# Optimization experiments

Hardware: AMD Instinct MI355X
Metric: run time of the kernel (lower is better)

The kernel has to match this reference:

```python
import jax, jax.numpy as jnp
import numpy as np

HID = 100  # LSTM hidden size (fixed in module)


def _lstm_final(x, Wih, Whh, bih, bhh, reverse):
    # x: [N, T, Hin]; returns final hidden state [N, HID] (PyTorch gate order i,f,g,o)
    xs = jnp.flip(x, axis=1) if reverse else x
    pre = jnp.einsum('nth,gh->ntg', xs, Wih) + bih + bhh  # [N, T, 4*HID]
    N = x.shape[0]
    h0 = jnp.zeros((N, HID), x.dtype)
    c0 = jnp.zeros((N, HID), x.dtype)

    def step(carry, pt):
        h, c = carry
        g = pt + h @ Whh.T
        i, f, gg, o = jnp.split(g, 4, axis=-1)
        c = jax.nn.sigmoid(f) * c + jax.nn.sigmoid(i) * jnp.tanh(gg)
        h = jax.nn.sigmoid(o) * jnp.tanh(c)
        return (h, c), None

    (h, c), _ = jax.lax.scan(step, (h0, c0), jnp.swapaxes(pre, 0, 1))
    return h


def setup_inputs():
    key = jax.random.key(0)
    ks = jax.random.split(key, 16)
    H, B, S, NP, PL = 768, 40, 128, 100, 20
    w = lambda k, shape: jax.random.normal(k, shape, jnp.float32) * 0.02
    return {
        'bert_output': jax.random.normal(ks[0], (B, S, H), jnp.float32),
        'commonsense': jax.random.normal(ks[1], (B * NP, PL, H), jnp.float32),
        'attention_mask': jnp.ones((B, S), jnp.int32),
        'commonsense_mask': jnp.ones((B, NP), jnp.int32),
        'b_size': 8, 'num_cand': 5, 'num_path': NP, 'path_len': PL,
        'lstm_Wih_f': w(ks[2], (4 * HID, H)), 'lstm_Whh_f': w(ks[3], (4 * HID, HID)),
        'lstm_bih_f': jnp.zeros((4 * HID,), jnp.float32), 'lstm_bhh_f': jnp.zeros((4 * HID,), jnp.float32),
        'lstm_Wih_b': w(ks[4], (4 * HID, H)), 'lstm_Whh_b': w(ks[5], (4 * HID, HID)),
        'lstm_bih_b': jnp.zeros((4 * HID,), jnp.float32), 'lstm_bhh_b': jnp.zeros((4 * HID,), jnp.float32),
        'proj_W': w(ks[6], (H, 2 * HID)), 'proj_b': jnp.zeros((H,), jnp.float32),
        'W1_w': w(ks[7], (1, H)), 'W1_b': jnp.zeros((1,), jnp.float32),
        'W2_w': w(ks[8], (1, H)), 'W2_b': jnp.zeros((1,), jnp.float32),
        'W3': w(ks[9], (1, 1, H)),
        'attp_W': w(ks[10], (H, 4 * H)), 'attp_b': jnp.zeros((H,), jnp.float32),
        'ln_w': jnp.ones((H,), jnp.float32), 'ln_b': jnp.zeros((H,), jnp.float32),
    }


def reference(bert_output, commonsense, attention_mask, commonsense_mask,
              b_size, num_cand, num_path, path_len,
              lstm_Wih_f, lstm_Whh_f, lstm_bih_f, lstm_bhh_f,
              lstm_Wih_b, lstm_Whh_b, lstm_bih_b, lstm_bhh_b,
              proj_W, proj_b, W1_w, W1_b, W2_w, W2_b, W3,
              attp_W, attp_b, ln_w, ln_b):
    Bc = b_size * num_cand
    # bidirectional LSTM over commonsense paths; only final hidden states are used
    h_f = _lstm_final(commonsense, lstm_Wih_f, lstm_Whh_f, lstm_bih_f, lstm_bhh_f, False)
    h_b = _lstm_final(commonsense, lstm_Wih_b, lstm_Whh_b, lstm_bih_b, lstm_bhh_b, True)
    enc = jnp.concatenate([h_f, h_b], axis=-1)               # [Bc*NP, 200]
    cs = jax.nn.relu(enc @ proj_W.T + proj_b).reshape(Bc, num_path, -1)  # [B, P, H]
    # trilinear BiDAF-style scores
    part1 = bert_output @ W1_w.T + W1_b                      # [B, S, 1]
    part2 = (cs @ W2_w.T + W2_b).transpose(0, 2, 1)          # [B, 1, P]
    part3 = jnp.einsum('bsh,bph->bsp', W3 * bert_output, cs)  # [B, S, P]
    mask_cs = (1.0 - commonsense_mask.astype(jnp.float32)) * -10000.0
    mask_dqa = (1.0 - attention_mask.astype(jnp.float32)) * -10000.0
    total = part1 + part2 + part3 + mask_cs[:, None, :] + mask_dqa[:, :, None]
    cs_att = jax.nn.softmax(total, axis=-1)                  # over paths
    weight_cs = jnp.einsum('bsp,bph->bsh', cs_att, cs)
    ctx_att = jax.nn.softmax(total, axis=1)                  # over context tokens
    probs = jnp.einsum('bsp,btp->bst', cs_att, ctx_att)      # [B, S, S]
    weighted_context = jnp.einsum('bst,bth->bsh', probs, bert_output)
    cat = jnp.concatenate([bert_output, weight_cs, bert_output * weight_cs,
                           bert_output * weighted_context], axis=-1)
    x = jax.nn.relu(cat @ attp_W.T + attp_b) + bert_output
    u = x.mean(-1, keepdims=True)
    s = ((x - u) ** 2).mean(-1, keepdims=True)
    return ln_w * ((x - u) / jnp.sqrt(s + 1e-12)) + ln_b
```

## Files before the change

### kernel.cpp

```cpp
#include <hip/hip_runtime.h>


typedef unsigned short ushort_t;
typedef unsigned int u32;
typedef __attribute__((ext_vector_type(8))) short short8;
typedef __attribute__((ext_vector_type(4))) float f32x4;
typedef __attribute__((address_space(1))) const u32 gu32;
typedef __attribute__((address_space(3))) u32 lu32;

__device__ __forceinline__ ushort_t f2bf(float f) {
  u32 x = __builtin_bit_cast(u32, f);
  u32 r = (x + 0x7fffu + ((x >> 16) & 1u)) >> 16;
  return (ushort_t)r;
}
__device__ __forceinline__ float bflo(u32 u) { return __builtin_bit_cast(float, u << 16); }
__device__ __forceinline__ float bfhi(u32 u) { return __builtin_bit_cast(float, u & 0xffff0000u); }
__device__ __forceinline__ u32 cvtpk(float lo, float hi) {
  u32 r;
  asm("v_cvt_pk_bf16_f32 %0, %1, %2" : "=v"(r) : "v"(lo), "v"(hi));
  return r;
}

__device__ __forceinline__ float sigm(float x) { return 1.f / (1.f + __expf(-x)); }
__device__ __forceinline__ float tanh_f(float x) { return 1.f - 2.f / (__expf(2.f * x) + 1.f); }


__global__ void prep_weights(const float* __restrict__ Wih_f, const float* __restrict__ Wih_b,
                             const float* __restrict__ Whh_f, const float* __restrict__ Whh_b,
                             const float* __restrict__ bih_f, const float* __restrict__ bhh_f,
                             const float* __restrict__ bih_b, const float* __restrict__ bhh_b,
                             const float* __restrict__ projW, const float* __restrict__ attpW,
                             ushort_t* __restrict__ wihcat, ushort_t* __restrict__ whhcat,
                             float* __restrict__ biascat, ushort_t* __restrict__ projw_bf,
                             ushort_t* __restrict__ attpw_bf) {
  const int TOT = 614400 + 102400 + 800 + 196608 + 2359296;
  for (int idx = blockIdx.x * 256 + threadIdx.x; idx < TOT; idx += gridDim.x * 256) {
    if (idx < 614400) {
      int g = idx / 768, k = idx % 768;
      float v = g < 400 ? Wih_f[g * 768 + k] : Wih_b[(g - 400) * 768 + k];
      wihcat[idx] = f2bf(v);
    } else if (idx < 716800) {
      int e = idx - 614400; int g = e / 128, j = e % 128;
      float v = 0.f;
      if (j < 100) v = g < 400 ? Whh_f[g * 100 + j] : Whh_b[(g - 400) * 100 + j];
      whhcat[e] = f2bf(v);
    } else if (idx < 717600) {
      int g = idx - 716800;
      biascat[g] = g < 400 ? bih_f[g] + bhh_f[g] : bih_b[g - 400] + bhh_b[g - 400];
    } else if (idx < 914208) {
      int e = idx - 717600; int o = e / 256, j = e % 256;
      float v = 0.f;
      if (j < 100) v = projW[o * 200 + j];
      else if (j >= 128 && j < 228) v = projW[o * 200 + 100 + (j - 128)];
      projw_bf[e] = f2bf(v);
    } else {
      int e = idx - 914208;
      attpw_bf[e] = f2bf(attpW[e]);
    }
  }
}

__global__ void convert_x_t(const float4* __restrict__ x4, ushort_t* __restrict__ xb) {
  for (int i = blockIdx.x * 256 + threadIdx.x; i < 15360000; i += gridDim.x * 256) {
    int seq = i / 3840;
    int rem = i - seq * 3840;
    int t = rem / 192;
    int k4 = rem - t * 192;
    float4 v = x4[i];
    ushort4 o;
    o.x = f2bf(v.x); o.y = f2bf(v.y); o.z = f2bf(v.z); o.w = f2bf(v.w);
    *reinterpret_cast<ushort4*>(&xb[((size_t)t * 4000 + seq) * 768 + k4 * 4]) = o;
  }
}

__global__ __launch_bounds__(256) void prep_bert(const float* __restrict__ bert,
                                                 const float* __restrict__ W3,
                                                 ushort_t* __restrict__ bw3,
                                                 ushort_t* __restrict__ bT,
                                                 ushort_t* __restrict__ cat) {
  __shared__ ushort_t tl[64 * 130];
  int ht = blockIdx.x, b = blockIdx.y;
  int h0 = ht * 64, tid = threadIdx.x;
  for (int e = tid; e < 8192; e += 256) {
    int t = e >> 6, hh = e & 63;
    float v = bert[((size_t)b * 128 + t) * 768 + h0 + hh];
    ushort_t vb = f2bf(v);
    bw3[((size_t)b * 128 + t) * 768 + h0 + hh] = f2bf(v * W3[h0 + hh]);
    cat[((size_t)b * 128 + t) * 3072 + h0 + hh] = vb;
    tl[hh * 130 + t] = vb;
  }
  __syncthreads();
  for (int e = tid; e < 8192; e += 256) {
    int hh = e >> 7, t = e & 127;
    bT[((size_t)b * 768 + h0 + hh) * 128 + t] = tl[hh * 130 + t];
  }
}

__global__ __launch_bounds__(256) void csT_k(const ushort_t* __restrict__ csb,
                                             ushort_t* __restrict__ csTcat) {
  __shared__ ushort_t tl[64 * 130];
  int ht = blockIdx.x, b = blockIdx.y;
  int h0 = ht * 64, tid = threadIdx.x;
  for (int e = tid; e < 6400; e += 256) {
    int p = e >> 6, hh = e & 63;
    tl[hh * 130 + p] = csb[((size_t)b * 100 + p) * 768 + h0 + hh];
  }
  __syncthreads();
  for (int e = tid; e < 8192; e += 256) {
    int hh = e >> 7, p = e & 127;
    csTcat[((size_t)b * 896 + h0 + hh) * 128 + p] = (p < 100) ? tl[hh * 130 + p] : (ushort_t)0;
  }
}


__global__ __launch_bounds__(256) void gemm_pre160(
    const ushort_t* __restrict__ A,
    const ushort_t* __restrict__ B,
    const float* __restrict__ bias,
    ushort_t* __restrict__ P)
{
  __shared__ __align__(16) ushort_t lsA[128 * 64];
  __shared__ __align__(16) ushort_t lsB[160 * 64];
  int bid = blockIdx.x;
  int xcd = bid & 7, slot = bid >> 3;
  int L = (xcd < 5) ? xcd * 391 + slot : 1955 + (xcd - 5) * 390 + slot;
  int bm = L / 5, bn = L - bm * 5;
  int m0 = bm * 128, n0 = bn * 160;
  int tid = threadIdx.x, lane = tid & 63, w = tid >> 6;
  int wr = w >> 1, wc = w & 1;
  int l15 = lane & 15, lk = lane >> 4;
  f32x4 acc[4][5];
  #pragma unroll
  for (int i = 0; i < 4; ++i)
    #pragma unroll
    for (int j = 0; j < 5; ++j)
      #pragma unroll
      for (int r = 0; r < 4; ++r) acc[i][j][r] = 0.f;

  int r_in = lane >> 3, p = lane & 7;
  for (int kt = 0; kt < 12; ++kt) {
    __syncthreads();
    #pragma unroll
    for (int i = 0; i < 4; ++i) {
      int seg = w * 4 + i;
      int row = seg * 8 + r_in;
      int sl = p ^ (row & 7);
      __builtin_amdgcn_global_load_lds(
          (gu32*)(A + (size_t)(m0 + row) * 768 + kt * 64 + sl * 8),
          (lu32*)(lsA + seg * 512), 16, 0, 0);
    }
    #pragma unroll
    for (int i = 0; i < 5; ++i) {
      int seg = w * 5 + i;
      int row = seg * 8 + r_in;
      int sl = p ^ (row & 7);
      __builtin_amdgcn_global_load_lds(
          (gu32*)(B + (size_t)(n0 + row) * 768 + kt * 64 + sl * 8),
          (lu32*)(lsB + seg * 512), 16, 0, 0);
    }
    __syncthreads();
    #pragma unroll
    for (int ks = 0; ks < 2; ++ks) {
      short8 af[4], bfv[5];
      #pragma unroll
      for (int f = 0; f < 4; ++f) {
        int row = wr * 64 + f * 16 + l15;
        af[f] = *reinterpret_cast<const short8*>(
            &lsA[row * 64 + (((ks * 4 + lk) ^ (row & 7)) << 3)]);
      }
      #pragma unroll
      for (int f = 0; f < 5; ++f) {
        int rowb = wc * 80 + f * 16 + l15;
        bfv[f] = *reinterpret_cast<const short8*>(
            &lsB[rowb * 64 + (((ks * 4 + lk) ^ (rowb & 7)) << 3)]);
      }
      #pragma unroll
      for (int fm = 0; fm < 4; ++fm)
        #pragma unroll
        for (int fn = 0; fn < 5; ++fn)
          acc[fm][fn] = __builtin_amdgcn_mfma_f32_16x16x32_bf16(af[fm], bfv[fn], acc[fm][fn], 0, 0, 0);
    }
  }
  #pragma unroll
  for (int fm = 0; fm < 4; ++fm) {
    int mb = m0 + wr * 64 + fm * 16;
    int t = mb / 4000;
    int sq = mb - t * 4000;
    int cch = sq >> 4;
    #pragma unroll
    for (int fn = 0; fn < 5; ++fn) {
      int nb = n0 + wc * 80 + fn * 16;
      int nl = nb < 400 ? nb : nb - 400;
      int nq = (nb < 400 ? 0 : 25) + (nl >> 4);
      float bsv = bias[nb + l15];
      uint2 pk;
      pk.x = cvtpk(acc[fm][fn][0] + bsv, acc[fm][fn][1] + bsv);
      pk.y = cvtpk(acc[fm][fn][2] + bsv, acc[fm][fn][3] + bsv);
      *reinterpret_cast<uint2*>(
          &P[((((size_t)t * 250 + cch) * 50 + nq) << 8) + l15 * 16 + lk * 4]) = pk;
    }
  }
}


__global__ __launch_bounds__(256) void gemm_proj(
    const ushort_t* __restrict__ A, int lda,
    const ushort_t* __restrict__ B, int ldb,
    int M, int N, int KT,
    const float* __restrict__ bias,
    float* __restrict__ C, int ldc,
    ushort_t* __restrict__ C2)
{
  __shared__ __align__(16) ushort_t lsA[128 * 64];
  __shared__ __align__(16) ushort_t lsB[128 * 64];
  int bm = blockIdx.x, bn = blockIdx.y;
  int m0 = bm * 128, n0 = bn * 128;
  int tid = threadIdx.x, lane = tid & 63, w = tid >> 6;
  int wr = w >> 1, wc = w & 1;
  int l15 = lane & 15, lk = lane >> 4;
  f32x4 acc[4][4];
  #pragma unroll
  for (int i = 0; i < 4; ++i)
    #pragma unroll
    for (int j = 0; j < 4; ++j)
      #pragma unroll
      for (int r = 0; r < 4; ++r) acc[i][j][r] = 0.f;

  int r_in = lane >> 3, p = lane & 7;
  for (int kt = 0; kt < KT; ++kt) {
    __syncthreads();
    #pragma unroll
    for (int i = 0; i < 4; ++i) {
      int seg = w * 4 + i;
      int row = seg * 8 + r_in;
      int sl = p ^ (row & 7);
      int m = m0 + row;
      if (m < M)
        __builtin_amdgcn_global_load_lds(
            (gu32*)(A + (size_t)m * lda + kt * 64 + sl * 8),
            (lu32*)(lsA + seg * 512), 16, 0, 0);
      int n = n0 + row;
      if (n < N)
        __builtin_amdgcn_global_load_lds(
            (gu32*)(B + (size_t)n * ldb + kt * 64 + sl * 8),
            (lu32*)(lsB + seg * 512), 16, 0, 0);
    }
    __syncthreads();
    #pragma unroll
    for (int ks = 0; ks < 2; ++ks) {
      short8 af[4], bfv[4];
      #pragma unroll
      for (int f = 0; f < 4; ++f) {
        int row = wr * 64 + f * 16 + l15;
        af[f] = *reinterpret_cast<const short8*>(
            &lsA[row * 64 + (((ks * 4 + lk) ^ (row & 7)) << 3)]);
        int rowb = wc * 64 + f * 16 + l15;
        bfv[f] = *reinterpret_cast<const short8*>(
            &lsB[rowb * 64 + (((ks * 4 + lk) ^ (rowb & 7)) << 3)]);
      }
      #pragma unroll
      for (int fm = 0; fm < 4; ++fm)
        #pragma unroll
        for (int fn = 0; fn < 4; ++fn)
          acc[fm][fn] = __builtin_amdgcn_mfma_f32_16x16x32_bf16(af[fm], bfv[fn], acc[fm][fn], 0, 0, 0);
    }
  }
  #pragma unroll
  for (int fm = 0; fm < 4; ++fm)
    #pragma unroll
    for (int fn = 0; fn < 4; ++fn)
      #pragma unroll
      for (int r = 0; r < 4; ++r) {
        int m = m0 + wr * 64 + fm * 16 + lk * 4 + r;
        int n = n0 + wc * 64 + fn * 16 + l15;
        if (m < M && n < N) {
          float v = fmaxf(acc[fm][fn][r] + bias[n], 0.f);
          C[(size_t)m * ldc + n] = v;
          C2[(size_t)m * ldc + n] = f2bf(v);
        }
      }
}


template <int EPI>
__global__ __launch_bounds__(256) void gemm128b(
    const ushort_t* __restrict__ A, long long sA, int lda,
    const ushort_t* __restrict__ Bm, long long sB, int ldb,
    int M, int N, int KT,
    float* __restrict__ Cf, ushort_t* __restrict__ Cb,
    const float* __restrict__ bertp, ushort_t* __restrict__ catp)
{
  __shared__ __align__(16) ushort_t lsA[128 * 64];
  __shared__ __align__(16) ushort_t lsB[128 * 64];
  int b = blockIdx.z;
  int koff = blockIdx.y * KT * 64;
  const ushort_t* Ab = A + (size_t)b * sA;
  const ushort_t* Bb = Bm + (size_t)b * sB;
  int n0 = blockIdx.x * 128;
  int tid = threadIdx.x, lane = tid & 63, w = tid >> 6;
  int wr = w >> 1, wc = w & 1;
  int l15 = lane & 15, lk = lane >> 4;
  f32x4 acc[4][4];
  #pragma unroll
  for (int i = 0; i < 4; ++i)
    #pragma unroll
    for (int j = 0; j < 4; ++j)
      #pragma unroll
      for (int r = 0; r < 4; ++r) acc[i][j][r] = 0.f;

  int r_in = lane >> 3, p = lane & 7;
  for (int kt = 0; kt < KT; ++kt) {
    __syncthreads();
    #pragma unroll
    for (int i = 0; i < 4; ++i) {
      int seg = w * 4 + i;
      int row = seg * 8 + r_in;
      int sl = p ^ (row & 7);
      if (row < M)
        __builtin_amdgcn_global_load_lds(
            (gu32*)(Ab + (size_t)row * lda + koff + kt * 64 + sl * 8),
            (lu32*)(lsA + seg * 512), 16, 0, 0);
      int n = n0 + row;
      if (n < N)
        __builtin_amdgcn_global_load_lds(
            (gu32*)(Bb + (size_t)n * ldb + koff + kt * 64 + sl * 8),
            (lu32*)(lsB + seg * 512), 16, 0, 0);
    }
    __syncthreads();
    #pragma unroll
    for (int ks = 0; ks < 2; ++ks) {
      short8 af[4], bfv[4];
      #pragma unroll
      for (int f = 0; f < 4; ++f) {
        int row = wr * 64 + f * 16 + l15;
        af[f] = *reinterpret_cast<const short8*>(
            &lsA[row * 64 + (((ks * 4 + lk) ^ (row & 7)) << 3)]);
        int rowb = wc * 64 + f * 16 + l15;
        bfv[f] = *reinterpret_cast<const short8*>(
            &lsB[rowb * 64 + (((ks * 4 + lk) ^ (rowb & 7)) << 3)]);
      }
      #pragma unroll
      for (int fm = 0; fm < 4; ++fm)
        #pragma unroll
        for (int fn = 0; fn < 4; ++fn)
          acc[fm][fn] = __builtin_amdgcn_mfma_f32_16x16x32_bf16(af[fm], bfv[fn], acc[fm][fn], 0, 0, 0);
    }
  }
  #pragma unroll
  for (int fm = 0; fm < 4; ++fm)
    #pragma unroll
    for (int fn = 0; fn < 4; ++fn)
      #pragma unroll
      for (int r = 0; r < 4; ++r) {
        int m = wr * 64 + fm * 16 + lk * 4 + r;
        int n = n0 + wc * 64 + fn * 16 + l15;
        if (m < M && n < N) {
          float v = acc[fm][fn][r];
          if (EPI == 10) {
            Cf[(size_t)blockIdx.y * 512000 + (size_t)b * 12800 + (size_t)m * 100 + n] = v;
          } else if (EPI == 12) {
            size_t row3 = ((size_t)b * 128 + m) * 3072;
            if (n < 768) {
              float bv = bertp[((size_t)b * 128 + m) * 768 + n];
              ushort_t wv = f2bf(v);
              catp[row3 + 768 + n] = wv;
              catp[row3 + 1536 + n] = f2bf(bv * bflo((u32)wv));
            } else {
              Cb[(size_t)b * 16384 + (size_t)m * 128 + (n - 768)] = f2bf(v);
            }
          } else {
            float bv = bertp[((size_t)b * 128 + m) * 768 + n];
            catp[((size_t)b * 128 + m) * 3072 + 2304 + n] = f2bf(bv * v);
          }
        }
      }
}


__global__ __launch_bounds__(256) void gemm64_attp(
    const ushort_t* __restrict__ A,
    const ushort_t* __restrict__ B,
    const float* __restrict__ bias,
    const float* __restrict__ resid,
    float* __restrict__ C)
{
  __shared__ __align__(16) ushort_t lsA[64 * 64];
  __shared__ __align__(16) ushort_t lsB[128 * 64];
  int bid = blockIdx.x;
  int xcd = bid & 7, slot = bid >> 3;
  int L = xcd * 60 + slot;
  int bm = L / 6, bn = L - bm * 6;
  int m0 = bm * 64, n0 = bn * 128;
  int tid = threadIdx.x, lane = tid & 63, w = tid >> 6;
  int wr = w >> 1, wc = w & 1;
  int l15 = lane & 15, lk = lane >> 4;
  f32x4 acc[2][4];
  #pragma unroll
  for (int i = 0; i < 2; ++i)
    #pragma unroll
    for (int j = 0; j < 4; ++j)
      #pragma unroll
      for (int r = 0; r < 4; ++r) acc[i][j][r] = 0.f;

  int r_in = lane >> 3, p = lane & 7;
  for (int kt = 0; kt < 48; ++kt) {
    __syncthreads();
    #pragma unroll
    for (int i = 0; i < 2; ++i) {
      int seg = w * 2 + i;
      int row = seg * 8 + r_in;
      int sl = p ^ (row & 7);
      __builtin_amdgcn_global_load_lds(
          (gu32*)(A + (size_t)(m0 + row) * 3072 + kt * 64 + sl * 8),
          (lu32*)(lsA + seg * 512), 16, 0, 0);
    }
    #pragma unroll
    for (int i = 0; i < 4; ++i) {
      int seg = w * 4 + i;
      int row = seg * 8 + r_in;
      int sl = p ^ (row & 7);
      __builtin_amdgcn_global_load_lds(
          (gu32*)(B + (size_t)(n0 + row) * 3072 + kt * 64 + sl * 8),
          (lu32*)(lsB + seg * 512), 16, 0, 0);
    }
    __syncthreads();
    #pragma unroll
    for (int ks = 0; ks < 2; ++ks) {
      short8 af[2], bfv[4];
      #pragma unroll
      for (int f = 0; f < 2; ++f) {
        int row = wr * 32 + f * 16 + l15;
        af[f] = *reinterpret_cast<const short8*>(
            &lsA[row * 64 + (((ks * 4 + lk) ^ (row & 7)) << 3)]);
      }
      #pragma unroll
      for (int f = 0; f < 4; ++f) {
        int rowb = wc * 64 + f * 16 + l15;
        bfv[f] = *reinterpret_cast<const short8*>(
            &lsB[rowb * 64 + (((ks * 4 + lk) ^ (rowb & 7)) << 3)]);
      }
      #pragma unroll
      for (int fm = 0; fm < 2; ++fm)
        #pragma unroll
        for (int fn = 0; fn < 4; ++fn)
          acc[fm][fn] = __builtin_amdgcn_mfma_f32_16x16x32_bf16(af[fm], bfv[fn], acc[fm][fn], 0, 0, 0);
    }
  }
  #pragma unroll
  for (int fm = 0; fm < 2; ++fm)
    #pragma unroll
    for (int fn = 0; fn < 4; ++fn)
      #pragma unroll
      for (int r = 0; r < 4; ++r) {
        int m = m0 + wr * 32 + fm * 16 + lk * 4 + r;
        int n = n0 + wc * 64 + fn * 16 + l15;
        float v = fmaxf(acc[fm][fn][r] + bias[n], 0.f) + resid[(size_t)m * 768 + n];
        C[(size_t)m * 768 + n] = v;
      }
}


__global__ __launch_bounds__(256) void lstm_recur(
    const ushort_t* __restrict__ pre,
    const ushort_t* __restrict__ whh,
    ushort_t* __restrict__ hcat)
{
  __shared__ __align__(16) ushort_t gx[25 * 256];
  __shared__ __align__(16) ushort_t h_lds[16 * 128];

  int dir = blockIdx.y;
  int c = blockIdx.x;
  int tid = threadIdx.x, lane = tid & 63, w = tid >> 6;
  int s = lane & 15, lk = lane >> 4;

  short8 wf[7][4];
  #pragma unroll
  for (int qi = 0; qi < 7; ++qi) {
    int q = w + qi * 4;
    if (q < 25) {
      const ushort_t* wp = whh + ((size_t)dir * 400 + q * 16 + s) * 128;
      #pragma unroll
      for (int ks = 0; ks < 4; ++ks)
        wf[qi][ks] = *reinterpret_cast<const short8*>(wp + ks * 32 + lk * 8);
    }
  }
  for (int e = tid; e < 1024; e += 256)
    *reinterpret_cast<u32*>(&h_lds[e * 2]) = 0u;

  float cst[2][4];
  #pragma unroll
  for (int g = 0; g < 2; ++g)
    #pragma unroll
    for (int r = 0; r < 4; ++r) cst[g][r] = 0.f;

  uint2 pvA[7], pvB[7];
  {
    int tt0 = dir ? 19 : 0;
    const ushort_t* pb = pre + ((((size_t)tt0 * 250 + c) * 50 + dir * 25) << 8);
    #pragma unroll
    for (int qi = 0; qi < 7; ++qi) {
      int q = w + qi * 4;
      if (q < 25) pvA[qi] = *reinterpret_cast<const uint2*>(pb + (q << 8) + s * 16 + lk * 4);
    }
  }
  __syncthreads();

  auto step = [&](uint2 (&pvc)[7], uint2 (&pvn)[7], int t) {
    f32x4 acc[7];
    #pragma unroll
    for (int qi = 0; qi < 7; ++qi)
      #pragma unroll
      for (int r = 0; r < 4; ++r) acc[qi][r] = 0.f;
    #pragma unroll
    for (int ks = 0; ks < 4; ++ks) {
      short8 af = *reinterpret_cast<const short8*>(
          &h_lds[s * 128 + (((ks * 4 + lk) ^ s) << 3)]);
      #pragma unroll
      for (int qi = 0; qi < 7; ++qi)
        if (w + qi * 4 < 25)
          acc[qi] = __builtin_amdgcn_mfma_f32_16x16x32_bf16(af, wf[qi][ks], acc[qi], 0, 0, 0);
    }
    #pragma unroll
    for (int qi = 0; qi < 7; ++qi)
      if (w + qi * 4 < 25) {
        acc[qi][0] += bflo(pvc[qi].x); acc[qi][1] += bfhi(pvc[qi].x);
        acc[qi][2] += bflo(pvc[qi].y); acc[qi][3] += bfhi(pvc[qi].y);
      }
    if (t + 1 < 20) {
      int tn = dir ? 19 - (t + 1) : (t + 1);
      const ushort_t* pb = pre + ((((size_t)tn * 250 + c) * 50 + dir * 25) << 8);
      #pragma unroll
      for (int qi = 0; qi < 7; ++qi) {
        int q = w + qi * 4;
        if (q < 25) pvn[qi] = *reinterpret_cast<const uint2*>(pb + (q << 8) + s * 16 + lk * 4);
      }
    }
    #pragma unroll
    for (int qi = 0; qi < 7; ++qi) {
      int q = w + qi * 4;
      if (q < 25) {
        ushort4 pk;
        pk.x = f2bf(acc[qi][0]); pk.y = f2bf(acc[qi][1]);
        pk.z = f2bf(acc[qi][2]); pk.w = f2bf(acc[qi][3]);
        *reinterpret_cast<ushort4*>(&gx[(q << 8) + s * 16 + lk * 4]) = pk;
      }
    }
    __syncthreads();
    #pragma unroll
    for (int gd = 0; gd < 2; ++gd) {
      int gi = w + gd * 4;
      if (gi < 7) {
        int j = gi * 16 + s;
        if (j < 100) {
          auto ld2 = [&](int q, int sp) {
            return *reinterpret_cast<const uint2*>(&gx[(q << 8) + sp * 16 + lk * 4]);
          };
          uint2 iv = ld2(gi, s);
          uint2 fv = (s < 12) ? ld2(6 + gi, s + 4) : ld2(7 + gi, s - 12);
          uint2 gv = (s < 8) ? ld2(12 + gi, s + 8) : ld2(13 + gi, s - 8);
          uint2 ov = (s < 4) ? ld2(18 + gi, s + 12) : ld2(19 + gi, s - 4);
          float ia[4] = {bflo(iv.x), bfhi(iv.x), bflo(iv.y), bfhi(iv.y)};
          float fa[4] = {bflo(fv.x), bfhi(fv.x), bflo(fv.y), bfhi(fv.y)};
          float ga[4] = {bflo(gv.x), bfhi(gv.x), bflo(gv.y), bfhi(gv.y)};
          float oa[4] = {bflo(ov.x), bfhi(ov.x), bflo(ov.y), bfhi(ov.y)};
          #pragma unroll
          for (int r = 0; r < 4; ++r) {
            float cc = sigm(fa[r]) * cst[gd][r] + sigm(ia[r]) * tanh_f(ga[r]);
            cst[gd][r] = cc;
            int row = lk * 4 + r;
            h_lds[row * 128 + (((j >> 3) ^ row) << 3) + (j & 7)] =
                f2bf(sigm(oa[r]) * tanh_f(cc));
          }
        }
      }
    }
    __syncthreads();
  };

  #pragma unroll 1
  for (int tp = 0; tp < 10; ++tp) {
    step(pvA, pvB, 2 * tp);
    step(pvB, pvA, 2 * tp + 1);
  }

  {
    int row = tid >> 4, sl = tid & 15;
    uint2 v = *reinterpret_cast<const uint2*>(&h_lds[row * 128 + ((sl ^ row) << 3)]);
    *reinterpret_cast<uint2*>(&hcat[(size_t)(c * 16 + row) * 256 + dir * 128 + sl * 8]) = v;
  }
}


__global__ void rowdot2(const float* __restrict__ bert, const float* __restrict__ cs,
                        const float* __restrict__ W1w, const float* __restrict__ W1b,
                        const float* __restrict__ W2w, const float* __restrict__ W2b,
                        float* __restrict__ part1, float* __restrict__ part2) {
  int row = blockIdx.x;
  int lane = threadIdx.x;
  const float* x;
  const float* wv;
  float b0;
  float* out;
  if (row < 5120) { x = bert + (size_t)row * 768; wv = W1w; b0 = W1b[0]; out = part1 + row; }
  else { int r = row - 5120; x = cs + (size_t)r * 768; wv = W2w; b0 = W2b[0]; out = part2 + r; }
  float s = 0.f;
  for (int k = lane; k < 768; k += 64) s += x[k] * wv[k];
  for (int off = 32; off; off >>= 1) s += __shfl_down(s, off);
  if (lane == 0) *out = s + b0;
}

__global__ void softmax_both(const float* __restrict__ t4,
                             const float* __restrict__ part1,
                             const float* __restrict__ part2,
                             const int* __restrict__ amask,
                             const int* __restrict__ cmask,
                             ushort_t* __restrict__ csatt,
                             ushort_t* __restrict__ csTcat) {
  int bid = blockIdx.x;
  int lane = threadIdx.x;
  auto tsum = [&](size_t idx) {
    return t4[idx] + t4[idx + 512000] + t4[idx + 1024000] + t4[idx + 1536000];
  };
  if (bid < 5120) {
    int b = bid >> 7;
    size_t base = (size_t)bid * 100;
    float e0 = tsum(base + lane) + part2[b * 100 + lane]
               + (1.f - (float)cmask[b * 100 + lane]) * -10000.f;
    bool has1 = (lane + 64) < 100;
    float e1 = -3.4e38f;
    if (has1)
      e1 = tsum(base + lane + 64) + part2[b * 100 + lane + 64]
           + (1.f - (float)cmask[b * 100 + lane + 64]) * -10000.f;
    float m = fmaxf(e0, e1);
    for (int off = 32; off; off >>= 1) m = fmaxf(m, __shfl_xor(m, off));
    float s0 = expf(e0 - m), s1 = has1 ? expf(e1 - m) : 0.f;
    float s = s0 + s1;
    for (int off = 32; off; off >>= 1) s += __shfl_xor(s, off);
    float inv = 1.f / s;
    csatt[(size_t)bid * 128 + lane] = f2bf(s0 * inv);
    csatt[(size_t)bid * 128 + lane + 64] = has1 ? f2bf(s1 * inv) : (ushort_t)0;
  } else {
    int idx = bid - 5120;
    int b = idx / 100, p = idx - b * 100;
    size_t base = (size_t)b * 12800 + p;
    int t0 = lane, t1 = lane + 64;
    float e0 = tsum(base + (size_t)t0 * 100) + part1[b * 128 + t0]
               + (1.f - (float)amask[b * 128 + t0]) * -10000.f;
    float e1 = tsum(base + (size_t)t1 * 100) + part1[b * 128 + t1]
               + (1.f - (float)amask[b * 128 + t1]) * -10000.f;
    float m = fmaxf(e0, e1);
    for (int off = 32; off; off >>= 1) m = fmaxf(m, __shfl_xor(m, off));
    float s0 = expf(e0 - m), s1 = expf(e1 - m);
    float s = s0 + s1;
    for (int off = 32; off; off >>= 1) s += __shfl_xor(s, off);
    float inv = 1.f / s;
    csTcat[((size_t)b * 896 + 768 + t0) * 128 + p] = f2bf(s0 * inv);
    csTcat[((size_t)b * 896 + 768 + t1) * 128 + p] = f2bf(s1 * inv);
  }
}

__global__ __launch_bounds__(256) void layernorm(float* __restrict__ X,
                                                 const float* __restrict__ w,
                                                 const float* __restrict__ bta) {
  int row = blockIdx.x;
  float* x = X + (size_t)row * 768;
  int t = threadIdx.x;
  float v[3];
  float s = 0.f;
  #pragma unroll
  for (int i = 0; i < 3; ++i) { v[i] = x[t + 256 * i]; s += v[i]; }
  __shared__ float red[256];
  red[t] = s; __syncthreads();
  for (int off = 128; off; off >>= 1) { if (t < off) red[t] += red[t + off]; __syncthreads(); }
  float mean = red[0] * (1.f / 768.f);
  __syncthreads();
  float q = 0.f;
  #pragma unroll
  for (int i = 0; i < 3; ++i) { float d = v[i] - mean; q += d * d; }
  red[t] = q; __syncthreads();
  for (int off = 128; off; off >>= 1) { if (t < off) red[t] += red[t + off]; __syncthreads(); }
  float inv = rsqrtf(red[0] * (1.f / 768.f) + 1e-12f);
  #pragma unroll
  for (int i = 0; i < 3; ++i) {
    int k = t + 256 * i;
    x[k] = w[k] * ((v[i] - mean) * inv) + bta[k];
  }
}


extern "C" void kernel_launch(void* const* d_in, const int* in_sizes, int n_in,
                              void* d_out, int out_size, void* d_ws, size_t ws_size,
                              hipStream_t stream) {
  (void)in_sizes; (void)n_in; (void)out_size; (void)ws_size;
  const float* bert  = (const float*)d_in[0];
  const float* cmn   = (const float*)d_in[1];
  const int*   amask = (const int*)d_in[2];
  const int*   cmask = (const int*)d_in[3];
  const float* Wih_f = (const float*)d_in[8];
  const float* Whh_f = (const float*)d_in[9];
  const float* bih_f = (const float*)d_in[10];
  const float* bhh_f = (const float*)d_in[11];
  const float* Wih_b = (const float*)d_in[12];
  const float* Whh_b = (const float*)d_in[13];
  const float* bih_b = (const float*)d_in[14];
  const float* bhh_b = (const float*)d_in[15];
  const float* projW = (const float*)d_in[16];
  const float* projb = (const float*)d_in[17];
  const float* W1w   = (const float*)d_in[18];
  const float* W1b   = (const float*)d_in[19];
  const float* W2w   = (const float*)d_in[20];
  const float* W2b   = (const float*)d_in[21];
  const float* W3    = (const float*)d_in[22];
  const float* attpW = (const float*)d_in[23];
  const float* attpb = (const float*)d_in[24];
  const float* lnw   = (const float*)d_in[25];
  const float* lnb   = (const float*)d_in[26];

  char* base = (char*)d_ws;
  size_t off = 0;
  auto alloc = [&](size_t bytes) -> char* {
    char* r = base + off;
    off += (bytes + 255) & ~(size_t)255;
    return r;
  };
  ushort_t* wihcat   = (ushort_t*)alloc(800 * 768 * 2);
  ushort_t* whhcat   = (ushort_t*)alloc(800 * 128 * 2);
  float*    biascat  = (float*)alloc(800 * 4);
  ushort_t* projw_bf = (ushort_t*)alloc(768 * 256 * 2);
  ushort_t* attpw_bf = (ushort_t*)alloc(768 * 3072 * 2);
  ushort_t* hcat     = (ushort_t*)alloc(4000 * 256 * 2);
  float*    cs       = (float*)alloc((size_t)4000 * 768 * 4);
  ushort_t* cs_bf    = (ushort_t*)alloc((size_t)4000 * 768 * 2);
  ushort_t* csTcat   = (ushort_t*)alloc((size_t)40 * 896 * 128 * 2);
  float*    part1    = (float*)alloc(5120 * 4);
  float*    part2    = (float*)alloc(4000 * 4);
  float*    total4   = (float*)alloc((size_t)4 * 40 * 128 * 100 * 4);
  ushort_t* csatt_bf = (ushort_t*)alloc((size_t)40 * 128 * 128 * 2);
  ushort_t* probs_bf = (ushort_t*)alloc((size_t)40 * 128 * 128 * 2);
  ushort_t* bw3_bf   = (ushort_t*)alloc((size_t)40 * 128 * 768 * 2);
  ushort_t* bertT    = (ushort_t*)alloc((size_t)40 * 768 * 128 * 2);
  ushort_t* cat      = (ushort_t*)alloc((size_t)5120 * 3072 * 2);
  ushort_t* x_bf     = (ushort_t*)alloc((size_t)20 * 4000 * 768 * 2);
  ushort_t* pre      = (ushort_t*)alloc((size_t)20 * 250 * 50 * 256 * 2);

  prep_weights<<<512, 256, 0, stream>>>(Wih_f, Wih_b, Whh_f, Whh_b, bih_f, bhh_f, bih_b, bhh_b,
                                        projW, attpW, wihcat, whhcat, biascat, projw_bf, attpw_bf);
  prep_bert<<<dim3(12, 40), 256, 0, stream>>>(bert, W3, bw3_bf, bertT, cat);
  convert_x_t<<<2048, 256, 0, stream>>>((const float4*)cmn, x_bf);

  gemm_pre160<<<3125, 256, 0, stream>>>(x_bf, wihcat, biascat, pre);
  lstm_recur<<<dim3(250, 2), 256, 0, stream>>>(pre, whhcat, hcat);

  gemm_proj<<<dim3(32, 6), 256, 0, stream>>>(hcat, 256, projw_bf, 256, 4000, 768, 4,
                                             projb, cs, 768, cs_bf);
  csT_k<<<dim3(12, 40), 256, 0, stream>>>(cs_bf, csTcat);
  rowdot2<<<9120, 64, 0, stream>>>(bert, cs, W1w, W1b, W2w, W2b, part1, part2);

  gemm128b<10><<<dim3(1, 4, 40), 256, 0, stream>>>(
      bw3_bf, 98304LL, 768, cs_bf, 76800LL, 768, 128, 100, 3,
      total4, nullptr, nullptr, nullptr);
  softmax_both<<<9120, 64, 0, stream>>>(total4, part1, part2, amask, cmask,
                                        csatt_bf, csTcat);
  gemm128b<12><<<dim3(7, 1, 40), 256, 0, stream>>>(
      csatt_bf, 16384LL, 128, csTcat, 114688LL, 128, 128, 896, 2,
      nullptr, probs_bf, bert, cat);
  gemm128b<13><<<dim3(6, 1, 40), 256, 0, stream>>>(
      probs_bf, 16384LL, 128, bertT, 98304LL, 128, 128, 768, 2,
      nullptr, nullptr, bert, cat);

  gemm64_attp<<<480, 256, 0, stream>>>(cat, attpw_bf, attpb, bert, (float*)d_out);
  layernorm<<<5120, 256, 0, stream>>>((float*)d_out, lnw, lnb);
}
```

Baseline: 497.4 us.

## Merge prep kernels, fuse cs transpose into proj GEMM, add occupancy bounds

Folds the weight conversion, bert prep, commonsense transpose-convert and the bert·W1 row-dot into one multi-role kernel launch, selected by block index. The separate csT transpose kernel is removed: the proj GEMM epilogue now writes the transposed bf16 copy directly. The remaining row-dot for cs packs four rows per block. The GEMM kernels get launch_bounds(256,4) to target higher occupancy. This cuts launch count and one full read of cs, at the cost of strided scattered stores in the GEMM epilogue and possible register spills from the occupancy hint. The zero padding in csTcat for columns 100–127 is no longer written.

```diff
diff --git a/kernel.cpp b/kernel.cpp
--- a/kernel.cpp
+++ b/kernel.cpp
@@ -25,95 +25,90 @@
 __device__ __forceinline__ float tanh_f(float x) { return 1.f - 2.f / (__expf(2.f * x) + 1.f); }
 
 
-__global__ void prep_weights(const float* __restrict__ Wih_f, const float* __restrict__ Wih_b,
-                             const float* __restrict__ Whh_f, const float* __restrict__ Whh_b,
-                             const float* __restrict__ bih_f, const float* __restrict__ bhh_f,
-                             const float* __restrict__ bih_b, const float* __restrict__ bhh_b,
-                             const float* __restrict__ projW, const float* __restrict__ attpW,
-                             ushort_t* __restrict__ wihcat, ushort_t* __restrict__ whhcat,
-                             float* __restrict__ biascat, ushort_t* __restrict__ projw_bf,
-                             ushort_t* __restrict__ attpw_bf) {
-  const int TOT = 614400 + 102400 + 800 + 196608 + 2359296;
-  for (int idx = blockIdx.x * 256 + threadIdx.x; idx < TOT; idx += gridDim.x * 256) {
-    if (idx < 614400) {
-      int g = idx / 768, k = idx % 768;
-      float v = g < 400 ? Wih_f[g * 768 + k] : Wih_b[(g - 400) * 768 + k];
-      wihcat[idx] = f2bf(v);
-    } else if (idx < 716800) {
-      int e = idx - 614400; int g = e / 128, j = e % 128;
-      float v = 0.f;
-      if (j < 100) v = g < 400 ? Whh_f[g * 100 + j] : Whh_b[(g - 400) * 100 + j];
-      whhcat[e] = f2bf(v);
-    } else if (idx < 717600) {
-      int g = idx - 716800;
-      biascat[g] = g < 400 ? bih_f[g] + bhh_f[g] : bih_b[g - 400] + bhh_b[g - 400];
-    } else if (idx < 914208) {
-      int e = idx - 717600; int o = e / 256, j = e % 256;
-      float v = 0.f;
-      if (j < 100) v = projW[o * 200 + j];
-      else if (j >= 128 && j < 228) v = projW[o * 200 + 100 + (j - 128)];
-      projw_bf[e] = f2bf(v);
-    } else {
-      int e = idx - 914208;
-      attpw_bf[e] = f2bf(attpW[e]);
-    }
-  }
-}
-
-__global__ void convert_x_t(const float4* __restrict__ x4, ushort_t* __restrict__ xb) {
-  for (int i = blockIdx.x * 256 + threadIdx.x; i < 15360000; i += gridDim.x * 256) {
-    int seq = i / 3840;
-    int rem = i - seq * 3840;
-    int t = rem / 192;
-    int k4 = rem - t * 192;
-    float4 v = x4[i];
-    ushort4 o;
-    o.x = f2bf(v.x); o.y = f2bf(v.y); o.z = f2bf(v.z); o.w = f2bf(v.w);
-    *reinterpret_cast<ushort4*>(&xb[((size_t)t * 4000 + seq) * 768 + k4 * 4]) = o;
-  }
-}
-
-__global__ __launch_bounds__(256) void prep_bert(const float* __restrict__ bert,
-                                                 const float* __restrict__ W3,
-                                                 ushort_t* __restrict__ bw3,
-                                                 ushort_t* __restrict__ bT,
-                                                 ushort_t* __restrict__ cat) {
+__global__ __launch_bounds__(256) void prep_all(
+    const float* __restrict__ Wih_f, const float* __restrict__ Wih_b,
+    const float* __restrict__ Whh_f, const float* __restrict__ Whh_b,
+    const float* __restrict__ bih_f, const float* __restrict__ bhh_f,
+    const float* __restrict__ bih_b, const float* __restrict__ bhh_b,
+    const float* __restrict__ projW, const float* __restrict__ attpW,
+    ushort_t* __restrict__ wihcat, ushort_t* __restrict__ whhcat,
+    float* __restrict__ biascat, ushort_t* __restrict__ projw_bf,
+    ushort_t* __restrict__ attpw_bf,
+    const float* __restrict__ bert, const float* __restrict__ W3,
+    ushort_t* __restrict__ bw3, ushort_t* __restrict__ bT, ushort_t* __restrict__ cat,
+    const float4* __restrict__ x4, ushort_t* __restrict__ xb,
+    const float* __restrict__ W1w, const float* __restrict__ W1b,
+    float* __restrict__ part1)
+{
   __shared__ ushort_t tl[64 * 130];
-  int ht = blockIdx.x, b = blockIdx.y;
-  int h0 = ht * 64, tid = threadIdx.x;
-  for (int e = tid; e < 8192; e += 256) {
-    int t = e >> 6, hh = e & 63;
-    float v = bert[((size_t)b * 128 + t) * 768 + h0 + hh];
-    ushort_t vb = f2bf(v);
-    bw3[((size_t)b * 128 + t) * 768 + h0 + hh] = f2bf(v * W3[h0 + hh]);
-    cat[((size_t)b * 128 + t) * 3072 + h0 + hh] = vb;
-    tl[hh * 130 + t] = vb;
-  }
-  __syncthreads();
-  for (int e = tid; e < 8192; e += 256) {
-    int hh = e >> 7, t = e & 127;
-    bT[((size_t)b * 768 + h0 + hh) * 128 + t] = tl[hh * 130 + t];
-  }
-}
-
-__global__ __launch_bounds__(256) void csT_k(const ushort_t* __restrict__ csb,
-                                             ushort_t* __restrict__ csTcat) {
-  __shared__ ushort_t tl[64 * 130];
-  int ht = blockIdx.x, b = blockIdx.y;
-  int h0 = ht * 64, tid = threadIdx.x;
-  for (int e = tid; e < 6400; e += 256) {
-    int p = e >> 6, hh = e & 63;
-    tl[hh * 130 + p] = csb[((size_t)b * 100 + p) * 768 + h0 + hh];
-  }
-  __syncthreads();
-  for (int e = tid; e < 8192; e += 256) {
-    int hh = e >> 7, p = e & 127;
-    csTcat[((size_t)b * 896 + h0 + hh) * 128 + p] = (p < 100) ? tl[hh * 130 + p] : (ushort_t)0;
-  }
-}
-
-
-__global__ __launch_bounds__(256) void gemm_pre160(
+  int bid = blockIdx.x, tid = threadIdx.x;
+  if (bid < 512) {
+    const int TOT = 614400 + 102400 + 800 + 196608 + 2359296;
+    for (int idx = bid * 256 + tid; idx < TOT; idx += 512 * 256) {
+      if (idx < 614400) {
+        int g = idx / 768, k = idx % 768;
+        float v = g < 400 ? Wih_f[g * 768 + k] : Wih_b[(g - 400) * 768 + k];
+        wihcat[idx] = f2bf(v);
+      } else if (idx < 716800) {
+        int e = idx - 614400; int g = e / 128, j = e % 128;
+        float v = 0.f;
+        if (j < 100) v = g < 400 ? Whh_f[g * 100 + j] : Whh_b[(g - 400) * 100 + j];
+        whhcat[e] = f2bf(v);
+      } else if (idx < 717600) {
+        int g = idx - 716800;
+        biascat[g] = g < 400 ? bih_f[g] + bhh_f[g] : bih_b[g - 400] + bhh_b[g - 400];
+      } else if (idx < 914208) {
+        int e = idx - 717600; int o = e / 256, j = e % 256;
+        float v = 0.f;
+        if (j < 100) v = projW[o * 200 + j];
+        else if (j >= 128 && j < 228) v = projW[o * 200 + 100 + (j - 128)];
+        projw_bf[e] = f2bf(v);
+      } else {
+        int e = idx - 914208;
+        attpw_bf[e] = f2bf(attpW[e]);
+      }
+    }
+  } else if (bid < 992) {
+    int e0 = bid - 512;
+    int ht = e0 % 12, b = e0 / 12;
+    int h0 = ht * 64;
+    for (int e = tid; e < 8192; e += 256) {
+      int t = e >> 6, hh = e & 63;
+      float v = bert[((size_t)b * 128 + t) * 768 + h0 + hh];
+      ushort_t vb = f2bf(v);
+      bw3[((size_t)b * 128 + t) * 768 + h0 + hh] = f2bf(v * W3[h0 + hh]);
+      cat[((size_t)b * 128 + t) * 3072 + h0 + hh] = vb;
+      tl[hh * 130 + t] = vb;
+    }
+    __syncthreads();
+    for (int e = tid; e < 8192; e += 256) {
+      int hh = e >> 7, t = e & 127;
+      bT[((size_t)b * 768 + h0 + hh) * 128 + t] = tl[hh * 130 + t];
+    }
+  } else if (bid < 3040) {
+    for (int i = (bid - 992) * 256 + tid; i < 15360000; i += 2048 * 256) {
+      int seq = i / 3840;
+      int rem = i - seq * 3840;
+      int t = rem / 192;
+      int k4 = rem - t * 192;
+      float4 v = x4[i];
+      ushort4 o;
+      o.x = f2bf(v.x); o.y = f2bf(v.y); o.z = f2bf(v.z); o.w = f2bf(v.w);
+      *reinterpret_cast<ushort4*>(&xb[((size_t)t * 4000 + seq) * 768 + k4 * 4]) = o;
+    }
+  } else {
+    int row = (bid - 3040) * 4 + (tid >> 6);
+    int lane = tid & 63;
+    const float* x = bert + (size_t)row * 768;
+    float s = 0.f;
+    for (int k = lane; k < 768; k += 64) s += x[k] * W1w[k];
+    for (int off = 32; off; off >>= 1) s += __shfl_down(s, off);
+    if (lane == 0) part1[row] = s + W1b[0];
+  }
+}
+
+
+__global__ __launch_bounds__(256, 4) void gemm_pre160(
     const ushort_t* __restrict__ A,
     const ushort_t* __restrict__ B,
     const float* __restrict__ bias,
@@ -203,13 +198,14 @@
 }
 
 
-__global__ __launch_bounds__(256) void gemm_proj(
+__global__ __launch_bounds__(256, 4) void gemm_proj(
     const ushort_t* __restrict__ A, int lda,
     const ushort_t* __restrict__ B, int ldb,
     int M, int N, int KT,
     const float* __restrict__ bias,
     float* __restrict__ C, int ldc,
-    ushort_t* __restrict__ C2)
+    ushort_t* __restrict__ C2,
+    ushort_t* __restrict__ csT)
 {
   __shared__ __align__(16) ushort_t lsA[128 * 64];
   __shared__ __align__(16) ushort_t lsB[128 * 64];
@@ -276,14 +272,17 @@
         if (m < M && n < N) {
           float v = fmaxf(acc[fm][fn][r] + bias[n], 0.f);
           C[(size_t)m * ldc + n] = v;
-          C2[(size_t)m * ldc + n] = f2bf(v);
+          ushort_t vb = f2bf(v);
+          C2[(size_t)m * ldc + n] = vb;
+          int bq = m / 100, pq = m - bq * 100;
+          csT[((size_t)bq * 896 + n) * 128 + pq] = vb;
         }
       }
 }
 
 
 template <int EPI>
-__global__ __launch_bounds__(256) void gemm128b(
+__global__ __launch_bounds__(256, 4) void gemm128b(
     const ushort_t* __restrict__ A, long long sA, int lda,
     const ushort_t* __restrict__ Bm, long long sB, int ldb,
     int M, int N, int KT,
@@ -377,7 +376,7 @@
 }
 
 
-__global__ __launch_bounds__(256) void gemm64_attp(
+__global__ __launch_bounds__(256, 4) void gemm64_attp(
     const ushort_t* __restrict__ A,
     const ushort_t* __restrict__ B,
     const float* __restrict__ bias,
@@ -591,22 +590,16 @@
 }
 
 
-__global__ void rowdot2(const float* __restrict__ bert, const float* __restrict__ cs,
-                        const float* __restrict__ W1w, const float* __restrict__ W1b,
-                        const float* __restrict__ W2w, const float* __restrict__ W2b,
-                        float* __restrict__ part1, float* __restrict__ part2) {
-  int row = blockIdx.x;
-  int lane = threadIdx.x;
-  const float* x;
-  const float* wv;
-  float b0;
-  float* out;
-  if (row < 5120) { x = bert + (size_t)row * 768; wv = W1w; b0 = W1b[0]; out = part1 + row; }
-  else { int r = row - 5120; x = cs + (size_t)r * 768; wv = W2w; b0 = W2b[0]; out = part2 + r; }
+__global__ void rowdot_cs(const float* __restrict__ cs,
+                          const float* __restrict__ W2w, const float* __restrict__ W2b,
+                          float* __restrict__ part2) {
+  int row = blockIdx.x * 4 + (threadIdx.x >> 6);
+  int lane = threadIdx.x & 63;
+  const float* x = cs + (size_t)row * 768;
   float s = 0.f;
-  for (int k = lane; k < 768; k += 64) s += x[k] * wv[k];
+  for (int k = lane; k < 768; k += 64) s += x[k] * W2w[k];
   for (int off = 32; off; off >>= 1) s += __shfl_down(s, off);
-  if (lane == 0) *out = s + b0;
+  if (lane == 0) part2[row] = s + W2b[0];
 }
 
 __global__ void softmax_both(const float* __restrict__ t4,
@@ -743,18 +736,19 @@
   ushort_t* x_bf     = (ushort_t*)alloc((size_t)20 * 4000 * 768 * 2);
   ushort_t* pre      = (ushort_t*)alloc((size_t)20 * 250 * 50 * 256 * 2);
 
-  prep_weights<<<512, 256, 0, stream>>>(Wih_f, Wih_b, Whh_f, Whh_b, bih_f, bhh_f, bih_b, bhh_b,
-                                        projW, attpW, wihcat, whhcat, biascat, projw_bf, attpw_bf);
-  prep_bert<<<dim3(12, 40), 256, 0, stream>>>(bert, W3, bw3_bf, bertT, cat);
-  convert_x_t<<<2048, 256, 0, stream>>>((const float4*)cmn, x_bf);
+  prep_all<<<4320, 256, 0, stream>>>(
+      Wih_f, Wih_b, Whh_f, Whh_b, bih_f, bhh_f, bih_b, bhh_b, projW, attpW,
+      wihcat, whhcat, biascat, projw_bf, attpw_bf,
+      bert, W3, bw3_bf, bertT, cat,
+      (const float4*)cmn, x_bf,
+      W1w, W1b, part1);
 
   gemm_pre160<<<3125, 256, 0, stream>>>(x_bf, wihcat, biascat, pre);
   lstm_recur<<<dim3(250, 2), 256, 0, stream>>>(pre, whhcat, hcat);
 
   gemm_proj<<<dim3(32, 6), 256, 0, stream>>>(hcat, 256, projw_bf, 256, 4000, 768, 4,
-                                             projb, cs, 768, cs_bf);
-  csT_k<<<dim3(12, 40), 256, 0, stream>>>(cs_bf, csTcat);
-  rowdot2<<<9120, 64, 0, stream>>>(bert, cs, W1w, W1b, W2w, W2b, part1, part2);
+                                             projb, cs, 768, cs_bf, csTcat);
+  rowdot_cs<<<1000, 256, 0, stream>>>(cs, W2w, W2b, part2);
 
   gemm128b<10><<<dim3(1, 4, 40), 256, 0, stream>>>(
       bw3_bf, 98304LL, 768, cs_bf, 76800LL, 768, 128, 100, 3,
```

Result: no change. 497.9 us (+0.1%).
